# Kernel optimization log

Hardware: AMD Instinct MI355X
Metric: run time of the kernel (lower is better)

The kernel has to match this reference:

```python
import jax, jax.numpy as jnp
import numpy as np

G = 251            # grid_size = int(1e6 ** 0.4)
ORDER = 3          # KAN_SPLINE_ORDER
NB = G + ORDER     # num_basis = 254
H = (1.05 - (-0.05)) / G
# grid: [-order .. G+order] * h + lo  -> length G + 2*ORDER + 1 = 258 (same for every feature)
GRID = jnp.arange(-ORDER, G + ORDER + 1, dtype=jnp.float32) * H + (-0.05)
EPS = 1e-8


def bsplines(x):
    # x: [B, in] -> bases: [B, in, NB] via Cox-de Boor recursion
    x = x[..., None]
    b = ((x >= GRID[:-1]) & (x < GRID[1:])).astype(x.dtype)
    for k in range(1, ORDER + 1):
        left = (x - GRID[:-(k + 1)]) / jnp.maximum(GRID[k:-1] - GRID[:-(k + 1)], EPS)
        right = (GRID[k + 1:] - x) / jnp.maximum(GRID[k + 1:] - GRID[1:-k], EPS)
        b = left * b[..., :-1] + right * b[..., 1:]
    return b


def kan_layer(x, bw, sw, wb, ws, residual):
    # base path: SiLU then linear
    base = jax.nn.silu(x) @ bw.T                      # [B, out]
    # spline path: basis [B, in*NB] @ spline_weight.reshape(out, in*NB).T
    bas = bsplines(x).reshape(x.shape[0], -1)
    spl = bas @ sw.reshape(sw.shape[0], -1).T         # [B, out]
    out = wb * base + ws * spl
    return out + x if residual else out


def setup_inputs() -> dict:
    key = jax.random.key(0)
    ks = jax.random.split(key, 20)
    B, D, W = 2048, 64, 256
    d = {"x": jax.random.uniform(ks[0], (B, D), dtype=jnp.float32)}
    dims = [(W, D), (W, W), (W, W), (1, W)]
    for i, (o, inp) in enumerate(dims):
        d[f"bw{i}"] = jax.random.normal(ks[1 + 4 * i], (o, inp), dtype=jnp.float32) * 0.05
        d[f"sw{i}"] = jax.random.normal(ks[2 + 4 * i], (o, inp, NB), dtype=jnp.float32) * (0.5 / G)
        d[f"wb{i}"] = jnp.ones((1,), jnp.float32)
        d[f"ws{i}"] = jnp.ones((1,), jnp.float32)
    return d


def reference(x, bw0, sw0, wb0, ws0, bw1, sw1, wb1, ws1, bw2, sw2, wb2, ws2, bw3, sw3, wb3, ws3):
    h = kan_layer(x, bw0, sw0, wb0, ws0, False)   # input layer, no residual (64 -> 256)
    h = kan_layer(h, bw1, sw1, wb1, ws1, True)    # hidden, residual (256 -> 256)
    h = kan_layer(h, bw2, sw2, wb2, ws2, True)    # hidden, residual (256 -> 256)
    return kan_layer(h, bw3, sw3, wb3, ws3, False)  # output layer (256 -> 1)
```

## Files before the change

### kernel.cpp

```cpp
#include <hip/hip_runtime.h>

#define BATCH 2048
#define NB 254

typedef float f4u __attribute__((ext_vector_type(4), aligned(4)));

__device__ __forceinline__ float selw(int pd, float w0, float w1, float w2, float w3) {
    return (pd == 0) ? w0 : (pd == 1) ? w1 : (pd == 2) ? w2 : (pd == 3) ? w3 : 0.f;
}

template<bool TR>
__global__ __launch_bounds__(256) void basis_kernel(
    const float* __restrict__ act, int IN,
    const float* __restrict__ wbp, const float* __restrict__ wsp,
    float2* __restrict__ sjbuf, float4* __restrict__ vbuf)
{
    int idx = blockIdx.x * 256 + threadIdx.x;
    int total = BATCH * IN;
    if (idx >= total) return;
    int i = idx / BATCH;
    int b = idx - i * BATCH;

    float x = TR ? act[idx] : act[(size_t)b * IN + i];
    float wb = wbp[0], wsc = wsp[0];

    float sil = x / (1.f + __expf(-x));

    const float LO = -0.05f;
    const float INVH = 228.18181818181818f;
    float uf = (x - LO) * INVH;
    float fm = floorf(uf);
    float t = uf - fm;
    int M = (int)fm + 3;

    bool valid = (M >= 0) && (M <= 256);

    float omt = 1.f - t;
    float t2 = t * t, t3 = t2 * t;
    const float S = 1.f / 6.f;
    float w0 = omt * omt * omt * S * wsc;
    float w1 = (3.f * t3 - 6.f * t2 + 4.f) * S * wsc;
    float w2 = (-3.f * t3 + 3.f * t2 + 3.f * t + 1.f) * S * wsc;
    float w3 = t3 * S * wsc;

    int js = M - 3;
    js = js < 0 ? 0 : js;
    js = js > (NB - 4) ? (NB - 4) : js;
    int d = js - (M - 3);

    float vp0 = selw(0 + d, w0, w1, w2, w3);
    float vp1 = selw(1 + d, w0, w1, w2, w3);
    float vp2 = selw(2 + d, w0, w1, w2, w3);
    float vp3 = selw(3 + d, w0, w1, w2, w3);

    if (!valid) js = -1;

    sjbuf[idx] = make_float2(sil * wb, __int_as_float(js));
    vbuf[idx] = make_float4(vp0, vp1, vp2, vp3);
}

template<int IN, int OT, bool RES, int IG, int BT>
__global__ __launch_bounds__(BT * IG) void accum_f32(
    const float2* __restrict__ sjbuf, const float4* __restrict__ vbuf,
    const float* __restrict__ bw, const float* __restrict__ sw,
    const float* __restrict__ resid, float* __restrict__ out)
{
    int bx = threadIdx.x;
    int g  = threadIdx.y;
    int b  = blockIdx.y * BT + bx;
    int o0 = blockIdx.x * OT;

    float acc[OT];
#pragma unroll
    for (int k = 0; k < OT; k++) acc[k] = 0.f;

    const size_t ostride = (size_t)IN * NB;
    const int CH = IN / IG;
    const int i0 = g * CH;

    for (int ii = 0; ii < CH; ii++) {
        int i = i0 + ii;
        float2 sj = sjbuf[i * BATCH + b];
        int j = __float_as_int(sj.y);
        float s = sj.x;
        const float* bq = bw + (size_t)o0 * IN + i;

#pragma unroll
        for (int oo = 0; oo < OT; oo++)
            acc[oo] += s * bq[oo * IN];

        if (j >= 0) {
            float4 v = vbuf[i * BATCH + b];
            const float* p = sw + (size_t)(o0 * IN + i) * NB + j;
            f4u wreg[OT];
#pragma unroll
            for (int oo = 0; oo < OT; oo++)
                wreg[oo] = *(const f4u*)(p + (size_t)oo * ostride);
#pragma unroll
            for (int oo = 0; oo < OT; oo++)
                acc[oo] += v.x * wreg[oo][0] + v.y * wreg[oo][1] + v.z * wreg[oo][2] + v.w * wreg[oo][3];
        }
    }

    __shared__ float lds[OT * (IG - 1) * BT];
    if (g > 0) {
#pragma unroll
        for (int oo = 0; oo < OT; oo++)
            lds[(oo * (IG - 1) + (g - 1)) * BT + bx] = acc[oo];
    }
    __syncthreads();
    if (g == 0) {
#pragma unroll
        for (int oo = 0; oo < OT; oo++) {
            float a = acc[oo];
            for (int gg = 1; gg < IG; gg++)
                a += lds[(oo * (IG - 1) + (gg - 1)) * BT + bx];
            size_t oidx = (size_t)(o0 + oo) * BATCH + b;
            float r = RES ? resid[oidx] : 0.f;
            out[oidx] = a + r;
        }
    }
}

__global__ __launch_bounds__(256) void out_kernel(
    const float2* __restrict__ sjbuf, const float4* __restrict__ vbuf,
    const float* __restrict__ bw, const float* __restrict__ sw,
    float* __restrict__ out)
{
    int tid = threadIdx.x;
    int bl = tid >> 6;
    int ig = tid & 63;
    int b = blockIdx.x * 4 + bl;

    float acc = 0.f;
    for (int ii = ig; ii < 256; ii += 64) {
        float2 sj = sjbuf[ii * BATCH + b];
        int j = __float_as_int(sj.y);
        acc += sj.x * bw[ii];
        if (j >= 0) {
            float4 v = vbuf[ii * BATCH + b];
            const float* p = sw + (size_t)ii * NB + j;
            acc += v.x * p[0] + v.y * p[1] + v.z * p[2] + v.w * p[3];
        }
    }
#pragma unroll
    for (int dlt = 32; dlt >= 1; dlt >>= 1) acc += __shfl_down(acc, dlt, 64);
    if (ig == 0) out[b] = acc;
}

extern "C" void kernel_launch(void* const* d_in, const int* in_sizes, int n_in,
                              void* d_out, int out_size, void* d_ws, size_t ws_size,
                              hipStream_t stream)
{
    const float* x   = (const float*)d_in[0];
    const float* bw0 = (const float*)d_in[1];
    const float* sw0 = (const float*)d_in[2];
    const float* wb0 = (const float*)d_in[3];
    const float* ws0 = (const float*)d_in[4];
    const float* bw1 = (const float*)d_in[5];
    const float* sw1 = (const float*)d_in[6];
    const float* wb1 = (const float*)d_in[7];
    const float* ws1 = (const float*)d_in[8];
    const float* bw2 = (const float*)d_in[9];
    const float* sw2 = (const float*)d_in[10];
    const float* wb2 = (const float*)d_in[11];
    const float* ws2 = (const float*)d_in[12];
    const float* bw3 = (const float*)d_in[13];
    const float* sw3 = (const float*)d_in[14];
    const float* wb3 = (const float*)d_in[15];
    const float* ws3 = (const float*)d_in[16];

    char* ws = (char*)d_ws;
    float4* vbuf  = (float4*)(ws);
    float2* sjbuf = (float2*)(ws + 8  * 1024 * 1024);
    float*  hA    = (float*)(ws + 12 * 1024 * 1024);
    float*  hB    = (float*)(ws + 14 * 1024 * 1024);

    float* out = (float*)d_out;

    dim3 ablk(64, 8);
    dim3 agrd(32, 32);

    basis_kernel<false><<<(BATCH * 64 + 255) / 256, 256, 0, stream>>>(x, 64, wb0, ws0, sjbuf, vbuf);
    accum_f32<64, 8, false, 8, 64><<<agrd, ablk, 0, stream>>>(sjbuf, vbuf, bw0, sw0, nullptr, hA);

    basis_kernel<true><<<(BATCH * 256 + 255) / 256, 256, 0, stream>>>(hA, 256, wb1, ws1, sjbuf, vbuf);
    accum_f32<256, 8, true, 8, 64><<<agrd, ablk, 0, stream>>>(sjbuf, vbuf, bw1, sw1, hA, hB);

    basis_kernel<true><<<(BATCH * 256 + 255) / 256, 256, 0, stream>>>(hB, 256, wb2, ws2, sjbuf, vbuf);
    accum_f32<256, 8, true, 8, 64><<<agrd, ablk, 0, stream>>>(sjbuf, vbuf, bw2, sw2, hB, hA);

    basis_kernel<true><<<(BATCH * 256 + 255) / 256, 256, 0, stream>>>(hA, 256, wb3, ws3, sjbuf, vbuf);
    out_kernel<<<BATCH / 4, 256, 0, stream>>>(sjbuf, vbuf, bw3, sw3, out);
}
```

Baseline: 285.1 us.

## Stage spline weight rows in double-buffered LDS for accumulation

```diff
diff --git a/kernel.cpp b/kernel.cpp
--- a/kernel.cpp
+++ b/kernel.cpp
@@ -2,8 +2,6 @@
 
 #define BATCH 2048
 #define NB 254
-
-typedef float f4u __attribute__((ext_vector_type(4), aligned(4)));
 
 __device__ __forceinline__ float selw(int pd, float w0, float w1, float w2, float w3) {
     return (pd == 0) ? w0 : (pd == 1) ? w1 : (pd == 2) ? w2 : (pd == 3) ? w3 : 0.f;
@@ -59,67 +57,67 @@
     vbuf[idx] = make_float4(vp0, vp1, vp2, vp3);
 }
 
-template<int IN, int OT, bool RES, int IG, int BT>
-__global__ __launch_bounds__(BT * IG) void accum_f32(
-    const float2* __restrict__ sjbuf, const float4* __restrict__ vbuf,
-    const float* __restrict__ bw, const float* __restrict__ sw,
-    const float* __restrict__ resid, float* __restrict__ out)
+template<int IN, bool RES>
+__global__ __launch_bounds__(1024) void accum_lds(
+    const float2* __restrict__ sjbuf,
+    const float4* __restrict__ vbuf,
+    const float* __restrict__ bw,
+    const float* __restrict__ sw,
+    const float* __restrict__ resid,
+    float* __restrict__ out)
 {
     int bx = threadIdx.x;
     int g  = threadIdx.y;
-    int b  = blockIdx.y * BT + bx;
-    int o0 = blockIdx.x * OT;
+    int b  = blockIdx.x * 128 + bx;
+    int o  = blockIdx.y * 8 + g;
 
-    float acc[OT];
-#pragma unroll
-    for (int k = 0; k < OT; k++) acc[k] = 0.f;
+    __shared__ float rows[2][8][256];
 
-    const size_t ostride = (size_t)IN * NB;
-    const int CH = IN / IG;
-    const int i0 = g * CH;
+    const float*  swrow = sw + (size_t)o * IN * NB;
+    const float*  bwp   = bw + (size_t)o * IN;
+    const float2* sjp   = sjbuf + b;
+    const float4* vvp   = vbuf + b;
 
-    for (int ii = 0; ii < CH; ii++) {
-        int i = i0 + ii;
-        float2 sj = sjbuf[i * BATCH + b];
+    if (bx < 127) {
+        float2 st = *(const float2*)(swrow + 2 * bx);
+        rows[0][g][2 * bx]     = st.x;
+        rows[0][g][2 * bx + 1] = st.y;
+    }
+    __syncthreads();
+
+    float acc = 0.f;
+
+    for (int i = 0; i < IN; i++) {
+        int cur = i & 1, nxt = cur ^ 1;
+
+        float2 nst;
+        bool do_stage = (i + 1 < IN) && (bx < 127);
+        if (do_stage)
+            nst = *(const float2*)(swrow + NB + 2 * bx);
+
+        float2 sj = sjp[(size_t)i * BATCH];
         int j = __float_as_int(sj.y);
-        float s = sj.x;
-        const float* bq = bw + (size_t)o0 * IN + i;
 
-#pragma unroll
-        for (int oo = 0; oo < OT; oo++)
-            acc[oo] += s * bq[oo * IN];
+        acc += sj.x * bwp[i];
 
         if (j >= 0) {
-            float4 v = vbuf[i * BATCH + b];
-            const float* p = sw + (size_t)(o0 * IN + i) * NB + j;
-            f4u wreg[OT];
-#pragma unroll
-            for (int oo = 0; oo < OT; oo++)
-                wreg[oo] = *(const f4u*)(p + (size_t)oo * ostride);
-#pragma unroll
-            for (int oo = 0; oo < OT; oo++)
-                acc[oo] += v.x * wreg[oo][0] + v.y * wreg[oo][1] + v.z * wreg[oo][2] + v.w * wreg[oo][3];
+            float4 v = vvp[(size_t)i * BATCH];
+            const float* rp = &rows[cur][g][0];
+            float t0 = rp[j], t1 = rp[j + 1], t2 = rp[j + 2], t3 = rp[j + 3];
+            acc += v.x * t0 + v.y * t1 + v.z * t2 + v.w * t3;
         }
+
+        if (do_stage) {
+            rows[nxt][g][2 * bx]     = nst.x;
+            rows[nxt][g][2 * bx + 1] = nst.y;
+        }
+        swrow += NB;
+        __syncthreads();
     }
 
-    __shared__ float lds[OT * (IG - 1) * BT];
-    if (g > 0) {
-#pragma unroll
-        for (int oo = 0; oo < OT; oo++)
-            lds[(oo * (IG - 1) + (g - 1)) * BT + bx] = acc[oo];
-    }
-    __syncthreads();
-    if (g == 0) {
-#pragma unroll
-        for (int oo = 0; oo < OT; oo++) {
-            float a = acc[oo];
-            for (int gg = 1; gg < IG; gg++)
-                a += lds[(oo * (IG - 1) + (gg - 1)) * BT + bx];
-            size_t oidx = (size_t)(o0 + oo) * BATCH + b;
-            float r = RES ? resid[oidx] : 0.f;
-            out[oidx] = a + r;
-        }
-    }
+    size_t oidx = (size_t)o * BATCH + b;
+    float r = RES ? resid[oidx] : 0.f;
+    out[oidx] = acc + r;
 }
 
 __global__ __launch_bounds__(256) void out_kernel(
@@ -178,17 +176,17 @@
 
     float* out = (float*)d_out;
 
-    dim3 ablk(64, 8);
-    dim3 agrd(32, 32);
+    dim3 ablk(128, 8);
+    dim3 agrd(16, 32);
 
     basis_kernel<false><<<(BATCH * 64 + 255) / 256, 256, 0, stream>>>(x, 64, wb0, ws0, sjbuf, vbuf);
-    accum_f32<64, 8, false, 8, 64><<<agrd, ablk, 0, stream>>>(sjbuf, vbuf, bw0, sw0, nullptr, hA);
+    accum_lds<64, false><<<agrd, ablk, 0, stream>>>(sjbuf, vbuf, bw0, sw0, nullptr, hA);
 
     basis_kernel<true><<<(BATCH * 256 + 255) / 256, 256, 0, stream>>>(hA, 256, wb1, ws1, sjbuf, vbuf);
-    accum_f32<256, 8, true, 8, 64><<<agrd, ablk, 0, stream>>>(sjbuf, vbuf, bw1, sw1, hA, hB);
+    accum_lds<256, true><<<agrd, ablk, 0, stream>>>(sjbuf, vbuf, bw1, sw1, hA, hB);
 
     basis_kernel<true><<<(BATCH * 256 + 255) / 256, 256, 0, stream>>>(hB, 256, wb2, ws2, sjbuf, vbuf);
-    accum_f32<256, 8, true, 8, 64><<<agrd, ablk, 0, stream>>>(sjbuf, vbuf, bw2, sw2, hB, hA);
+    accum_lds<256, true><<<agrd, ablk, 0, stream>>>(sjbuf, vbuf, bw2, sw2, hB, hA);
 
     basis_kernel<true><<<(BATCH * 256 + 255) / 256, 256, 0, stream>>>(hA, 256, wb3, ws3, sjbuf, vbuf);
     out_kernel<<<BATCH / 4, 256, 0, stream>>>(sjbuf, vbuf, bw3, sw3, out);
```

After: 621.5 us. +118.0%, slower.

## Fuse B-spline basis computation into accumulation kernels for hidden and output layers

Applied to the files above, without the earlier changes.

```diff
diff --git a/kernel.cpp b/kernel.cpp
--- a/kernel.cpp
+++ b/kernel.cpp
@@ -9,22 +9,11 @@
     return (pd == 0) ? w0 : (pd == 1) ? w1 : (pd == 2) ? w2 : (pd == 3) ? w3 : 0.f;
 }
 
-template<bool TR>
-__global__ __launch_bounds__(256) void basis_kernel(
-    const float* __restrict__ act, int IN,
-    const float* __restrict__ wbp, const float* __restrict__ wsp,
-    float2* __restrict__ sjbuf, float4* __restrict__ vbuf)
-{
-    int idx = blockIdx.x * 256 + threadIdx.x;
-    int total = BATCH * IN;
-    if (idx >= total) return;
-    int i = idx / BATCH;
-    int b = idx - i * BATCH;
-
-    float x = TR ? act[idx] : act[(size_t)b * IN + i];
-    float wb = wbp[0], wsc = wsp[0];
-
-    float sil = x / (1.f + __expf(-x));
+__device__ __forceinline__ void basis_math(
+    float x, float wsc, float& sil, int& js,
+    float& vp0, float& vp1, float& vp2, float& vp3)
+{
+    sil = x / (1.f + __expf(-x));
 
     const float LO = -0.05f;
     const float INVH = 228.18181818181818f;
@@ -43,17 +32,35 @@
     float w2 = (-3.f * t3 + 3.f * t2 + 3.f * t + 1.f) * S * wsc;
     float w3 = t3 * S * wsc;
 
-    int js = M - 3;
+    js = M - 3;
     js = js < 0 ? 0 : js;
     js = js > (NB - 4) ? (NB - 4) : js;
     int d = js - (M - 3);
 
-    float vp0 = selw(0 + d, w0, w1, w2, w3);
-    float vp1 = selw(1 + d, w0, w1, w2, w3);
-    float vp2 = selw(2 + d, w0, w1, w2, w3);
-    float vp3 = selw(3 + d, w0, w1, w2, w3);
+    vp0 = selw(0 + d, w0, w1, w2, w3);
+    vp1 = selw(1 + d, w0, w1, w2, w3);
+    vp2 = selw(2 + d, w0, w1, w2, w3);
+    vp3 = selw(3 + d, w0, w1, w2, w3);
 
     if (!valid) js = -1;
+}
+
+__global__ __launch_bounds__(256) void basis_kernel(
+    const float* __restrict__ act, int IN,
+    const float* __restrict__ wbp, const float* __restrict__ wsp,
+    float2* __restrict__ sjbuf, float4* __restrict__ vbuf)
+{
+    int idx = blockIdx.x * 256 + threadIdx.x;
+    int total = BATCH * IN;
+    if (idx >= total) return;
+    int i = idx / BATCH;
+    int b = idx - i * BATCH;
+
+    float x = act[(size_t)b * IN + i];
+    float wb = wbp[0], wsc = wsp[0];
+
+    float sil; int js; float vp0, vp1, vp2, vp3;
+    basis_math(x, wsc, sil, js, vp0, vp1, vp2, vp3);
 
     sjbuf[idx] = make_float2(sil * wb, __int_as_float(js));
     vbuf[idx] = make_float4(vp0, vp1, vp2, vp3);
@@ -122,30 +129,108 @@
     }
 }
 
-__global__ __launch_bounds__(256) void out_kernel(
-    const float2* __restrict__ sjbuf, const float4* __restrict__ vbuf,
+template<int IN, int OT, int IG, int BT>
+__global__ __launch_bounds__(BT * IG) void fused_accum(
+    const float* __restrict__ act,
+    const float* __restrict__ wbp, const float* __restrict__ wsp,
     const float* __restrict__ bw, const float* __restrict__ sw,
     float* __restrict__ out)
 {
-    int tid = threadIdx.x;
-    int bl = tid >> 6;
-    int ig = tid & 63;
-    int b = blockIdx.x * 4 + bl;
-
+    int bx = threadIdx.x;
+    int g  = threadIdx.y;
+    int b  = blockIdx.y * BT + bx;
+    int o0 = blockIdx.x * OT;
+
+    float wb = wbp[0], wsc = wsp[0];
+
+    float acc[OT];
+#pragma unroll
+    for (int k = 0; k < OT; k++) acc[k] = 0.f;
+
+    const size_t ostride = (size_t)IN * NB;
+    const int CH = IN / IG;
+    const int i0 = g * CH;
+
+    for (int ii = 0; ii < CH; ii++) {
+        int i = i0 + ii;
+        float x = act[(size_t)i * BATCH + b];
+
+        float sil; int j; float vp0, vp1, vp2, vp3;
+        basis_math(x, wsc, sil, j, vp0, vp1, vp2, vp3);
+        float s = sil * wb;
+
+        const float* bq = bw + (size_t)o0 * IN + i;
+#pragma unroll
+        for (int oo = 0; oo < OT; oo++)
+            acc[oo] += s * bq[oo * IN];
+
+        if (j >= 0) {
+            const float* p = sw + (size_t)(o0 * IN + i) * NB + j;
+            f4u wreg[OT];
+#pragma unroll
+            for (int oo = 0; oo < OT; oo++)
+                wreg[oo] = *(const f4u*)(p + (size_t)oo * ostride);
+#pragma unroll
+            for (int oo = 0; oo < OT; oo++)
+                acc[oo] += vp0 * wreg[oo][0] + vp1 * wreg[oo][1] + vp2 * wreg[oo][2] + vp3 * wreg[oo][3];
+        }
+    }
+
+    __shared__ float lds[OT * (IG - 1) * BT];
+    if (g > 0) {
+#pragma unroll
+        for (int oo = 0; oo < OT; oo++)
+            lds[(oo * (IG - 1) + (g - 1)) * BT + bx] = acc[oo];
+    }
+    __syncthreads();
+    if (g == 0) {
+#pragma unroll
+        for (int oo = 0; oo < OT; oo++) {
+            float a = acc[oo];
+            for (int gg = 1; gg < IG; gg++)
+                a += lds[(oo * (IG - 1) + (gg - 1)) * BT + bx];
+            size_t oidx = (size_t)(o0 + oo) * BATCH + b;
+            out[oidx] = a + act[oidx];
+        }
+    }
+}
+
+__global__ __launch_bounds__(1024) void out_fused(
+    const float* __restrict__ act,
+    const float* __restrict__ wbp, const float* __restrict__ wsp,
+    const float* __restrict__ bw, const float* __restrict__ sw,
+    float* __restrict__ out)
+{
+    int lane = threadIdx.x & 63;
+    int w    = threadIdx.x >> 6;
+    int b    = blockIdx.x * 64 + lane;
+
+    float wb = wbp[0], wsc = wsp[0];
     float acc = 0.f;
-    for (int ii = ig; ii < 256; ii += 64) {
-        float2 sj = sjbuf[ii * BATCH + b];
-        int j = __float_as_int(sj.y);
-        acc += sj.x * bw[ii];
+
+#pragma unroll 4
+    for (int k = 0; k < 16; k++) {
+        int i = w * 16 + k;
+        float x = act[(size_t)i * BATCH + b];
+
+        float sil; int j; float vp0, vp1, vp2, vp3;
+        basis_math(x, wsc, sil, j, vp0, vp1, vp2, vp3);
+
+        acc += sil * wb * bw[i];
         if (j >= 0) {
-            float4 v = vbuf[ii * BATCH + b];
-            const float* p = sw + (size_t)ii * NB + j;
-            acc += v.x * p[0] + v.y * p[1] + v.z * p[2] + v.w * p[3];
-        }
-    }
-#pragma unroll
-    for (int dlt = 32; dlt >= 1; dlt >>= 1) acc += __shfl_down(acc, dlt, 64);
-    if (ig == 0) out[b] = acc;
+            const float* p = sw + (size_t)i * NB + j;
+            acc += vp0 * p[0] + vp1 * p[1] + vp2 * p[2] + vp3 * p[3];
+        }
+    }
+
+    __shared__ float red[16][64];
+    red[w][lane] = acc;
+    __syncthreads();
+    if (w == 0) {
+        float a = acc;
+        for (int k = 1; k < 16; k++) a += red[k][lane];
+        out[b] = a;
+    }
 }
 
 extern "C" void kernel_launch(void* const* d_in, const int* in_sizes, int n_in,
@@ -181,15 +266,12 @@
     dim3 ablk(64, 8);
     dim3 agrd(32, 32);
 
-    basis_kernel<false><<<(BATCH * 64 + 255) / 256, 256, 0, stream>>>(x, 64, wb0, ws0, sjbuf, vbuf);
+    basis_kernel<<<(BATCH * 64 + 255) / 256, 256, 0, stream>>>(x, 64, wb0, ws0, sjbuf, vbuf);
     accum_f32<64, 8, false, 8, 64><<<agrd, ablk, 0, stream>>>(sjbuf, vbuf, bw0, sw0, nullptr, hA);
 
-    basis_kernel<true><<<(BATCH * 256 + 255) / 256, 256, 0, stream>>>(hA, 256, wb1, ws1, sjbuf, vbuf);
-    accum_f32<256, 8, true, 8, 64><<<agrd, ablk, 0, stream>>>(sjbuf, vbuf, bw1, sw1, hA, hB);
-
-    basis_kernel<true><<<(BATCH * 256 + 255) / 256, 256, 0, stream>>>(hB, 256, wb2, ws2, sjbuf, vbuf);
-    accum_f32<256, 8, true, 8, 64><<<agrd, ablk, 0, stream>>>(sjbuf, vbuf, bw2, sw2, hB, hA);
-
-    basis_kernel<true><<<(BATCH * 256 + 255) / 256, 256, 0, stream>>>(hA, 256, wb3, ws3, sjbuf, vbuf);
-    out_kernel<<<BATCH / 4, 256, 0, stream>>>(sjbuf, vbuf, bw3, sw3, out);
-}
+    fused_accum<256, 8, 8, 64><<<agrd, ablk, 0, stream>>>(hA, wb1, ws1, bw1, sw1, hB);
+
+    fused_accum<256, 8, 8, 64><<<agrd, ablk, 0, stream>>>(hB, wb2, ws2, bw2, sw2, hA);
+
+    out_fused<<<BATCH / 64, 1024, 0, stream>>>(hA, wb3, ws3, bw3, sw3, out);
+}
```

After: 257.4 us. 1.11x faster.
